# Kernel tuning notes

Measured on AMD Instinct MI355X. Metric: run time of the kernel, lower is better.

Reference implementation:

```python
import jax, jax.numpy as jnp
import numpy as np

EPS = 1e-12  # torch F.normalize eps


def setup_inputs() -> dict:
    key = jax.random.key(0)
    k1, k2, k3 = jax.random.split(key, 3)
    N, C, H, W = 64, 512, 30, 30
    K = 64
    x = jax.random.normal(k1, (N, C, H, W), dtype=jnp.float32)
    # 1x1 conv weight [K, C] (kernel spatial dims squeezed out)
    conv_w = jax.random.normal(k2, (K, C), dtype=jnp.float32) * 0.04
    centroids = jax.random.uniform(k3, (K, C), dtype=jnp.float32)
    return {"x": x, "conv_w": conv_w, "centroids": centroids}


def reference(x, conv_w, centroids):
    N, C, H, W = x.shape
    K = conv_w.shape[0]
    # descriptor-wise L2 normalize over channel dim (normalize_input=True)
    nrm = jnp.sqrt(jnp.sum(x * x, axis=1, keepdims=True))
    x = x / jnp.maximum(nrm, EPS)
    xf = x.reshape(N, C, H * W)                       # [N, C, P]
    # 1x1 conv == per-pixel matmul: [N, K, P]
    logits = jnp.einsum("kc,ncp->nkp", conv_w, xf)
    a = jax.nn.softmax(logits, axis=1)                # softmax over clusters
    # vlad[n,k,c] = sum_p a[n,k,p] * (xf[n,c,p] - centroids[k,c])
    #            = (a @ xf^T) - sum_p(a) * centroids   (GEMM decomposition)
    agg = jnp.einsum("nkp,ncp->nkc", a, xf)           # [N, K, C]
    vlad = agg - a.sum(axis=-1)[:, :, None] * centroids[None]
    return vlad
```

## Files before the change

### kernel.cpp

```cpp
#include <hip/hip_runtime.h>
#include <math.h>

#define N_DIM 64
#define C_DIM 512
#define K_DIM 64
#define P_DIM 900
#define P_PAD 928
#define PTILES 15

typedef __attribute__((ext_vector_type(8))) short short8;
typedef __attribute__((ext_vector_type(4))) float f32x4;
typedef __attribute__((ext_vector_type(4))) uint  u32x4;

#define A2_ELEMS   ((size_t)N_DIM * K_DIM * P_PAD)

__device__ inline ushort f2bf(float f) {
  uint u = __builtin_bit_cast(uint, f);
  u += 0x7FFFu + ((u >> 16) & 1u);
  return (ushort)(u >> 16);
}
__device__ inline uint pk2(float a, float b) {
  return (uint)f2bf(a) | ((uint)f2bf(b) << 16);
}

__global__ __launch_bounds__(256, 2) void netvlad_assign(
    const float* __restrict__ x, const float* __restrict__ w,
    ushort* __restrict__ a2, float* __restrict__ asum_part)
{
  const int n = blockIdx.y, bpt = blockIdx.x, p0 = bpt * 64;
  const int tid = threadIdx.x, wave = tid >> 6, lane = tid & 63;
  const int l15 = lane & 15, lhi = lane >> 4;

  __shared__ float wredm[4][4][16];
  __shared__ float wreds[4][4][16];

  short8 wfrag[16];
  const float* wrow = w + (size_t)(wave * 16 + l15) * C_DIM + lhi * 8;
#pragma unroll
  for (int ks = 0; ks < 16; ++ks) {
    f32x4 f0 = *(const f32x4*)(wrow + ks * 32);
    f32x4 f1 = *(const f32x4*)(wrow + ks * 32 + 4);
    u32x4 up;
    up[0] = pk2(f0[0], f0[1]); up[1] = pk2(f0[2], f0[3]);
    up[2] = pk2(f1[0], f1[1]); up[3] = pk2(f1[2], f1[3]);
    wfrag[ks] = __builtin_bit_cast(short8, up);
  }

  const float* xb = x + (size_t)n * C_DIM * P_DIM;
  int pb = p0 + 4 * l15;
  if (pb > P_DIM - 4) pb = P_DIM - 4;
  const float* xbase = xb + pb + (size_t)(lhi * 8) * P_DIM;

  f32x4 acc[4];
#pragma unroll
  for (int pt = 0; pt < 4; ++pt) acc[pt] = (f32x4){0.f, 0.f, 0.f, 0.f};
  float ssqp[4] = {0.f, 0.f, 0.f, 0.f};

#pragma unroll
  for (int ks = 0; ks < 16; ++ks) {
    const float* src = xbase + (size_t)(ks * 32) * P_DIM;
    f32x4 xv0 = *(const f32x4*)(src + 0 * P_DIM);
    f32x4 xv1 = *(const f32x4*)(src + 1 * P_DIM);
    f32x4 xv2 = *(const f32x4*)(src + 2 * P_DIM);
    f32x4 xv3 = *(const f32x4*)(src + 3 * P_DIM);
    f32x4 xv4 = *(const f32x4*)(src + 4 * P_DIM);
    f32x4 xv5 = *(const f32x4*)(src + 5 * P_DIM);
    f32x4 xv6 = *(const f32x4*)(src + 6 * P_DIM);
    f32x4 xv7 = *(const f32x4*)(src + 7 * P_DIM);
#pragma unroll
    for (int pt = 0; pt < 4; ++pt) {
      ssqp[pt] += xv0[pt] * xv0[pt] + xv1[pt] * xv1[pt]
                + xv2[pt] * xv2[pt] + xv3[pt] * xv3[pt]
                + xv4[pt] * xv4[pt] + xv5[pt] * xv5[pt]
                + xv6[pt] * xv6[pt] + xv7[pt] * xv7[pt];
      u32x4 up;
      up[0] = pk2(xv0[pt], xv1[pt]); up[1] = pk2(xv2[pt], xv3[pt]);
      up[2] = pk2(xv4[pt], xv5[pt]); up[3] = pk2(xv6[pt], xv7[pt]);
      short8 xf = __builtin_bit_cast(short8, up);
      acc[pt] = __builtin_amdgcn_mfma_f32_16x16x32_bf16(wfrag[ks], xf, acc[pt], 0, 0, 0);
    }
  }

  float linv[4];
#pragma unroll
  for (int pt = 0; pt < 4; ++pt) {
    float s = ssqp[pt];
    s += __shfl_xor(s, 16);
    s += __shfl_xor(s, 32);
    linv[pt] = 1.0f / fmaxf(sqrtf(s), 1e-12f);
  }

  float lg[4][4];
#pragma unroll
  for (int pt = 0; pt < 4; ++pt) {
    float m = -1e30f;
#pragma unroll
    for (int r = 0; r < 4; ++r) { lg[pt][r] = acc[pt][r] * linv[pt]; m = fmaxf(m, lg[pt][r]); }
    m = fmaxf(m, __shfl_xor(m, 16));
    m = fmaxf(m, __shfl_xor(m, 32));
    if (lhi == 0) wredm[wave][pt][l15] = m;
  }
  __syncthreads();
#pragma unroll
  for (int pt = 0; pt < 4; ++pt) {
    float m = fmaxf(fmaxf(wredm[0][pt][l15], wredm[1][pt][l15]),
                    fmaxf(wredm[2][pt][l15], wredm[3][pt][l15]));
    float s = 0.f;
#pragma unroll
    for (int r = 0; r < 4; ++r) { lg[pt][r] = __expf(lg[pt][r] - m); s += lg[pt][r]; }
    s += __shfl_xor(s, 16);
    s += __shfl_xor(s, 32);
    if (lhi == 0) wreds[wave][pt][l15] = s;
  }
  __syncthreads();

  ushort* a2b = a2 + (size_t)n * K_DIM * P_PAD;
  float asr[4] = {0.f, 0.f, 0.f, 0.f};
#pragma unroll
  for (int pt = 0; pt < 4; ++pt) {
    float stot = wreds[0][pt][l15] + wreds[1][pt][l15] +
                 wreds[2][pt][l15] + wreds[3][pt][l15];
    float rs = 1.0f / stot;
    int p = p0 + 4 * l15 + pt;
    bool vv = p < P_DIM;
#pragma unroll
    for (int r = 0; r < 4; ++r) {
      float a = lg[pt][r] * rs;
      if (vv) asr[r] += a;
      if (p < P_PAD) {
        int k = wave * 16 + lhi * 4 + r;
        a2b[(size_t)k * P_PAD + p] = vv ? f2bf(a * linv[pt]) : (ushort)0;
      }
    }
  }
#pragma unroll
  for (int r = 0; r < 4; ++r) {
    float v = asr[r];
    v += __shfl_xor(v, 1); v += __shfl_xor(v, 2);
    v += __shfl_xor(v, 4); v += __shfl_xor(v, 8);
    if (l15 == 0) {
      int k = wave * 16 + lhi * 4 + r;
      asum_part[((size_t)n * K_DIM + k) * PTILES + bpt] = v;
    }
  }
}

__global__ __launch_bounds__(256, 4) void netvlad_agg(
    const float* __restrict__ x, const ushort* __restrict__ a2,
    const float* __restrict__ asum_part, const float* __restrict__ cent,
    float* __restrict__ out)
{
  const int n = blockIdx.y, ct = blockIdx.x, c0 = ct * 64;
  const int tid = threadIdx.x, wave = tid >> 6, lane = tid & 63;
  const int l15 = lane & 15, lhi = lane >> 4;

  __shared__ float asum_s[64];
  if (tid < 64) {
    const float* ap = asum_part + ((size_t)n * K_DIM + tid) * PTILES;
    float s = 0.f;
#pragma unroll
    for (int j = 0; j < PTILES; ++j) s += ap[j];
    asum_s[tid] = s;
  }
  __syncthreads();

  f32x4 acc[4];
#pragma unroll
  for (int mt = 0; mt < 4; ++mt) acc[mt] = (f32x4){0.f, 0.f, 0.f, 0.f};

  const float*  xrow = x + (size_t)n * C_DIM * P_DIM
                         + (size_t)(c0 + wave * 16 + l15) * P_DIM;
  const ushort* ab   = a2 + (size_t)n * K_DIM * P_PAD;

  for (int ks = 0; ks < 29; ++ks) {
    int pb = ks * 32 + lhi * 8;
    short8 bfrag;
    if (pb + 8 <= P_DIM) {
      f32x4 f0 = *(const f32x4*)(xrow + pb);
      f32x4 f1 = *(const f32x4*)(xrow + pb + 4);
      u32x4 up;
      up[0] = pk2(f0[0], f0[1]); up[1] = pk2(f0[2], f0[3]);
      up[2] = pk2(f1[0], f1[1]); up[3] = pk2(f1[2], f1[3]);
      bfrag = __builtin_bit_cast(short8, up);
    } else {
#pragma unroll
      for (int j = 0; j < 8; ++j)
        bfrag[j] = (pb + j < P_DIM) ? (short)f2bf(xrow[pb + j]) : (short)0;
    }
#pragma unroll
    for (int mt = 0; mt < 4; ++mt) {
      short8 afrag = *(const short8*)(ab + (size_t)(mt * 16 + l15) * P_PAD
                                         + ks * 32 + lhi * 8);
      acc[mt] = __builtin_amdgcn_mfma_f32_16x16x32_bf16(afrag, bfrag, acc[mt], 0, 0, 0);
    }
  }

  const int c = c0 + wave * 16 + l15;
#pragma unroll
  for (int mt = 0; mt < 4; ++mt) {
#pragma unroll
    for (int r = 0; r < 4; ++r) {
      int k = mt * 16 + lhi * 4 + r;
      out[((size_t)n * K_DIM + k) * C_DIM + c] =
          acc[mt][r] - asum_s[k] * cent[(size_t)k * C_DIM + c];
    }
  }
}

extern "C" void kernel_launch(void* const* d_in, const int* in_sizes, int n_in,
                              void* d_out, int out_size, void* d_ws, size_t ws_size,
                              hipStream_t stream) {
  const float* x    = (const float*)d_in[0];
  const float* w    = (const float*)d_in[1];
  const float* cent = (const float*)d_in[2];
  float* out = (float*)d_out;

  ushort* a2        = (ushort*)d_ws;
  float*  asum_part = (float*)((char*)d_ws + A2_ELEMS * sizeof(ushort));

  netvlad_assign<<<dim3(PTILES, N_DIM), 256, 0, stream>>>(x, w, a2, asum_part);
  netvlad_agg   <<<dim3(8, N_DIM),      256, 0, stream>>>(x, a2, asum_part, cent, out);
}
```

Measured before the change: 83.90 us.

## Pre-transpose x into bf16 MFMA-fragment layout in a separate kernel

Adds a transpose kernel that stages x rows into LDS via global_load_lds and writes a bf16 copy laid out exactly as the MFMA B-fragments the assign kernel consumes. The assign kernel then does one contiguous 16-byte load per fragment instead of eight strided fp32 loads plus conversion, and it computes the norm from the bf16 values. The aim is to remove strided, poorly coalesced global reads in the assign stage. The cost is an extra launch, an extra write and read of a bf16 copy of x, and a norm that is now computed at reduced precision.

Measured after the change: 93.13 us. +11.0%, slower.

```diff
diff --git a/kernel.cpp b/kernel.cpp
--- a/kernel.cpp
+++ b/kernel.cpp
@@ -13,6 +13,8 @@
 typedef __attribute__((ext_vector_type(4))) uint  u32x4;
 
 #define A2_ELEMS   ((size_t)N_DIM * K_DIM * P_PAD)
+#define ASUM_ELEMS ((size_t)N_DIM * K_DIM * PTILES)
+#define XTF_ELEMS  ((size_t)N_DIM * PTILES * 16 * 4 * 512)
 
 __device__ inline ushort f2bf(float f) {
   uint u = __builtin_bit_cast(uint, f);
@@ -22,9 +24,49 @@
 __device__ inline uint pk2(float a, float b) {
   return (uint)f2bf(a) | ((uint)f2bf(b) << 16);
 }
+__device__ __forceinline__ void gload16(const float* g, float* lds_base) {
+  __builtin_amdgcn_global_load_lds(
+      (const __attribute__((address_space(1))) void*)g,
+      (__attribute__((address_space(3))) void*)lds_base, 16, 0, 0);
+}
+
+__global__ __launch_bounds__(256, 4) void transpose_x(
+    const float* __restrict__ x, ushort* __restrict__ xtf)
+{
+  const int oct = blockIdx.x, n = blockIdx.y;
+  const int tid = threadIdx.x, wv = tid >> 6, lane = tid & 63;
+  __shared__ float lds[8][1024];
+
+  const float* xb = x + ((size_t)n * C_DIM + oct * 8) * P_DIM;
+#pragma unroll
+  for (int i = 0; i < 8; ++i) {
+    int j = wv * 8 + i;
+    int r = j >> 2, q = j & 3;
+    int pxb = (q == 3) ? 644 : q * 256;
+    gload16(xb + (size_t)r * P_DIM + pxb + lane * 4, &lds[r][pxb]);
+  }
+  __syncthreads();
+
+  const int ks = oct >> 2, lhi = oct & 3;
+#pragma unroll
+  for (int j = 0; j < 4; ++j) {
+    int px = j * 256 + tid;
+    float v[8];
+#pragma unroll
+    for (int c = 0; c < 8; ++c) v[c] = (px < P_DIM) ? lds[c][px] : 0.f;
+    if (px < PTILES * 64) {
+      int pt = px >> 6, pxl = px & 63;
+      u32x4 wvr;
+      wvr[0] = pk2(v[0], v[1]); wvr[1] = pk2(v[2], v[3]);
+      wvr[2] = pk2(v[4], v[5]); wvr[3] = pk2(v[6], v[7]);
+      *(u32x4*)(xtf + ((((size_t)(n * PTILES + pt) * 16 + ks) * 4 + lhi) * 64
+                       + pxl) * 8) = wvr;
+    }
+  }
+}
 
 __global__ __launch_bounds__(256, 2) void netvlad_assign(
-    const float* __restrict__ x, const float* __restrict__ w,
+    const float* __restrict__ w, const ushort* __restrict__ xtf,
     ushort* __restrict__ a2, float* __restrict__ asum_part)
 {
   const int n = blockIdx.y, bpt = blockIdx.x, p0 = bpt * 64;
@@ -46,11 +88,7 @@
     wfrag[ks] = __builtin_bit_cast(short8, up);
   }
 
-  const float* xb = x + (size_t)n * C_DIM * P_DIM;
-  int pb = p0 + 4 * l15;
-  if (pb > P_DIM - 4) pb = P_DIM - 4;
-  const float* xbase = xb + pb + (size_t)(lhi * 8) * P_DIM;
-
+  const ushort* xf_base = xtf + ((size_t)(n * PTILES + bpt) * 16) * 4 * 512;
   f32x4 acc[4];
 #pragma unroll
   for (int pt = 0; pt < 4; ++pt) acc[pt] = (f32x4){0.f, 0.f, 0.f, 0.f};
@@ -58,25 +96,17 @@
 
 #pragma unroll
   for (int ks = 0; ks < 16; ++ks) {
-    const float* src = xbase + (size_t)(ks * 32) * P_DIM;
-    f32x4 xv0 = *(const f32x4*)(src + 0 * P_DIM);
-    f32x4 xv1 = *(const f32x4*)(src + 1 * P_DIM);
-    f32x4 xv2 = *(const f32x4*)(src + 2 * P_DIM);
-    f32x4 xv3 = *(const f32x4*)(src + 3 * P_DIM);
-    f32x4 xv4 = *(const f32x4*)(src + 4 * P_DIM);
-    f32x4 xv5 = *(const f32x4*)(src + 5 * P_DIM);
-    f32x4 xv6 = *(const f32x4*)(src + 6 * P_DIM);
-    f32x4 xv7 = *(const f32x4*)(src + 7 * P_DIM);
 #pragma unroll
     for (int pt = 0; pt < 4; ++pt) {
-      ssqp[pt] += xv0[pt] * xv0[pt] + xv1[pt] * xv1[pt]
-                + xv2[pt] * xv2[pt] + xv3[pt] * xv3[pt]
-                + xv4[pt] * xv4[pt] + xv5[pt] * xv5[pt]
-                + xv6[pt] * xv6[pt] + xv7[pt] * xv7[pt];
-      u32x4 up;
-      up[0] = pk2(xv0[pt], xv1[pt]); up[1] = pk2(xv2[pt], xv3[pt]);
-      up[2] = pk2(xv4[pt], xv5[pt]); up[3] = pk2(xv6[pt], xv7[pt]);
-      short8 xf = __builtin_bit_cast(short8, up);
+      short8 xf = *(const short8*)(xf_base + ((size_t)ks * 4 + lhi) * 512
+                                          + (pt * 16 + l15) * 8);
+      u32x4 uw = __builtin_bit_cast(u32x4, xf);
+#pragma unroll
+      for (int wd = 0; wd < 4; ++wd) {
+        float lo = __builtin_bit_cast(float, uw[wd] << 16);
+        float hi = __builtin_bit_cast(float, uw[wd] & 0xffff0000u);
+        ssqp[pt] += lo * lo + hi * hi;
+      }
       acc[pt] = __builtin_amdgcn_mfma_f32_16x16x32_bf16(wfrag[ks], xf, acc[pt], 0, 0, 0);
     }
   }
@@ -121,7 +151,7 @@
     float stot = wreds[0][pt][l15] + wreds[1][pt][l15] +
                  wreds[2][pt][l15] + wreds[3][pt][l15];
     float rs = 1.0f / stot;
-    int p = p0 + 4 * l15 + pt;
+    int p = p0 + pt * 16 + l15;
     bool vv = p < P_DIM;
 #pragma unroll
     for (int r = 0; r < 4; ++r) {
@@ -215,9 +245,12 @@
   const float* cent = (const float*)d_in[2];
   float* out = (float*)d_out;
 
-  ushort* a2        = (ushort*)d_ws;
-  float*  asum_part = (float*)((char*)d_ws + A2_ELEMS * sizeof(ushort));
-
-  netvlad_assign<<<dim3(PTILES, N_DIM), 256, 0, stream>>>(x, w, a2, asum_part);
+  char* wsb = (char*)d_ws;
+  ushort* a2        = (ushort*)wsb;
+  float*  asum_part = (float*)(wsb + A2_ELEMS * sizeof(ushort));
+  ushort* xtf       = (ushort*)((char*)(asum_part + ASUM_ELEMS));
+
+  transpose_x   <<<dim3(64, N_DIM),     256, 0, stream>>>(x, xtf);
+  netvlad_assign<<<dim3(PTILES, N_DIM), 256, 0, stream>>>(w, xtf, a2, asum_part);
   netvlad_agg   <<<dim3(8, N_DIM),      256, 0, stream>>>(x, a2, asum_part, cent, out);
 }
```
